# Performance work log

Hardware: AMD Instinct MI355X
Metric: run time of the kernel (lower is better)

The kernel has to match this reference:

```python
import jax, jax.numpy as jnp
import numpy as np


def setup_inputs() -> dict:
    key = jax.random.key(0)
    k1, k2 = jax.random.split(key)
    B, D, T = 32, 128, 1024   # batch, emb_dim, time (bdt layout)
    K = 4096                  # emb_size (codebook entries)
    x = jax.random.normal(k1, (B, D, T), dtype=jnp.float32)
    # nn.Embedding weight, init uniform(-1/K, 1/K) in the original; scale irrelevant for correctness
    W = jax.random.normal(k2, (K, D), dtype=jnp.float32) * (1.0 / K)
    return {"x": x, "W": W}


def reference(x, W):
    # Quantizer.forward with bdt_flag=True, eval mode (no EMA buffer update).
    # x: [B, D, T], W: [K, D] codebook
    xt = jnp.transpose(x, (0, 2, 1))            # [B, T, D]
    B, T, D = xt.shape
    flat = xt.reshape(-1, D)                    # [N, D]
    dist = (jnp.sum(W * W, axis=1)
            - 2.0 * flat @ W.T
            + jnp.sum(flat * flat, axis=1, keepdims=True))
    qidx = jnp.argmin(dist, axis=1).reshape(B, T)          # [B, T] int
    embed_idx = jnp.take(W, qidx, axis=0)                  # [B, T, D] == onehot @ W
    # straight-through estimator
    embed_idx_qx = xt + jax.lax.stop_gradient(embed_idx - xt)
    embed_idx_qx = jnp.transpose(embed_idx_qx, (0, 2, 1))  # back to [B, D, T]
    return embed_idx, embed_idx_qx, qidx
```

## Files before the change

kernel.cpp:

```cpp
#include <hip/hip_runtime.h>

typedef float    f4 __attribute__((ext_vector_type(4)));
typedef float    f2 __attribute__((ext_vector_type(2)));
typedef _Float16 h8 __attribute__((ext_vector_type(8)));

#define B_ 32
#define D_ 128
#define T_ 1024
#define K_ 4096
#define NROWS (B_ * T_)
#define LPX 132
#define INF_ 3.4e38f

#define SCHED_FENCE() __builtin_amdgcn_sched_barrier(0)
#define MFMA16 __builtin_amdgcn_mfma_f32_16x16x32_f16

__device__ __forceinline__ float opaquef(float x) { asm volatile("" : "+v"(x)); return x; }

__device__ float np_sumsq128(const float* a) {
  float r[8];
#pragma unroll
  for (int j = 0; j < 8; ++j) r[j] = opaquef(a[j] * a[j]);
#pragma unroll
  for (int i = 8; i < 128; i += 8) {
#pragma unroll
    for (int j = 0; j < 8; ++j) r[j] = r[j] + opaquef(a[i + j] * a[i + j]);
  }
  return ((r[0] + r[1]) + (r[2] + r[3])) + ((r[4] + r[5]) + (r[6] + r[7]));
}

__global__ void wsq_kernel(const float* __restrict__ W, float* __restrict__ wsq,
                           unsigned* __restrict__ maxwsq) {
  int k = blockIdx.x * blockDim.x + threadIdx.x;
  if (k < K_) {
    float s = np_sumsq128(W + (size_t)k * D_);
    wsq[k] = s;
    atomicMax(maxwsq, __float_as_uint(s));
  }
}

__global__ void wbf_prep_kernel(const float* __restrict__ W, _Float16* __restrict__ Wbf) {
  int e = blockIdx.x * 256 + threadIdx.x;
  int j = e & 7, lane = (e >> 3) & 63, kk = (e >> 9) & 3, ct = e >> 11;
  int code = (ct << 4) + (lane & 15);
  int k = (kk << 5) + (((lane >> 4) & 3) << 3) + j;
  Wbf[e] = (_Float16)(W[(size_t)code * D_ + k] * 4096.0f);
}

#define LDB(R0, R1, R2, R3, WQ)               \
  R0 = *(const h8*)(pwb);                     \
  R1 = *(const h8*)(pwb + 1024);              \
  R2 = *(const h8*)(pwb + 2048);              \
  R3 = *(const h8*)(pwb + 3072);              \
  WQ = *pwq;                                  \
  pwb += 4096; pwq += 16;

#define TOP3_UPD(T, J, U, KK)                                                  \
  do {                                                                         \
    bool c1 = (U) < m1[T][J], c2 = (U) < m2[T][J];                             \
    m3[T][J] = __builtin_amdgcn_fmed3f((U), m2[T][J], m3[T][J]);               \
    m2[T][J] = __builtin_amdgcn_fmed3f((U), m1[T][J], m2[T][J]);               \
    m1[T][J] = fminf((U), m1[T][J]);                                           \
    i2[T][J] = c1 ? i1[T][J] : (c2 ? (KK) : i2[T][J]);                         \
    i1[T][J] = c1 ? (KK) : i1[T][J];                                           \
  } while (0)

#define CONSUME_MIN(B0, B1, B2, B3, WQ, CT)                                    \
  do {                                                                         \
    f4 z = {0.f, 0.f, 0.f, 0.f};                                               \
    f4 A0 = MFMA16(afr0[0], B0, z, 0, 0, 0);                                   \
    A0 = MFMA16(afr0[1], B1, A0, 0, 0, 0);                                     \
    f4 A1 = MFMA16(afr0[2], B2, z, 0, 0, 0);                                   \
    A1 = MFMA16(afr0[3], B3, A1, 0, 0, 0);                                     \
    f4 C0 = MFMA16(afr1[0], B0, z, 0, 0, 0);                                   \
    C0 = MFMA16(afr1[1], B1, C0, 0, 0, 0);                                     \
    f4 C1 = MFMA16(afr1[2], B2, z, 0, 0, 0);                                   \
    C1 = MFMA16(afr1[3], B3, C1, 0, 0, 0);                                     \
    const int kk_ = ((CT) << 4) + cidx;                                        \
    _Pragma("unroll")                                                          \
    for (int j = 0; j < 4; ++j) {                                              \
      float u0 = __fmaf_rn(-4.8828125e-4f, A0[j] + A1[j], WQ);                 \
      TOP3_UPD(0, j, u0, kk_);                                                 \
      float u1 = __fmaf_rn(-4.8828125e-4f, C0[j] + C1[j], WQ);                 \
      TOP3_UPD(1, j, u1, kk_);                                                 \
    }                                                                          \
  } while (0)

__global__ __launch_bounds__(256) void filter_kernel(
    const float* __restrict__ x, const _Float16* __restrict__ Wbf,
    const float* __restrict__ wsq, const unsigned* __restrict__ maxwsq,
    float* __restrict__ xsq_g, int* __restrict__ cnt, int* __restrict__ cand,
    int* __restrict__ flags, int* __restrict__ nflag, int* __restrict__ flist) {
  __shared__ float xs[32][LPX];
  __shared__ float xsqs[32];
  __shared__ float umin_sh[32][4];
  const int tid = threadIdx.x;
  const int blkrow = blockIdx.x * 32;
  const int b = blockIdx.x >> 5, t0 = (blockIdx.x & 31) << 5;

  {
    int tt = tid & 31, d0 = (tid >> 5) * 16;
    for (int dd = 0; dd < 16; ++dd) {
      int d = d0 + dd;
      xs[tt][d] = x[((size_t)b * D_ + d) * T_ + t0 + tt];
    }
  }
  __syncthreads();
  if (tid < 32) {
    float s = np_sumsq128(&xs[tid][0]);
    xsqs[tid] = s;
    xsq_g[blkrow + tid] = s;
  }
  __syncthreads();

  const int w = tid >> 6, lane = tid & 63;
  const int cidx = lane & 15;
  const int q = lane >> 4;

  h8 afr0[4], afr1[4];
#pragma unroll
  for (int kk = 0; kk < 4; ++kk)
#pragma unroll
    for (int j = 0; j < 8; ++j) {
      int k = (kk << 5) + (q << 3) + j;
      afr0[kk][j] = (_Float16)xs[cidx][k];
      afr1[kk][j] = (_Float16)xs[16 + cidx][k];
    }

  const float mw = sqrtf(__uint_as_float(*maxwsq)) * 1.0001f;

  float m1[2][4], m2[2][4], m3[2][4];
  int   i1[2][4], i2[2][4];
#pragma unroll
  for (int t = 0; t < 2; ++t)
#pragma unroll
    for (int j = 0; j < 4; ++j) {
      m1[t][j] = INF_; m2[t][j] = INF_; m3[t][j] = INF_;
      i1[t][j] = 0x7fffffff; i2[t][j] = 0x7fffffff;
    }
  const int ct0 = w << 6;

  {
    const char*  pwb = (const char*)Wbf + (size_t)ct0 * 4096 + (size_t)lane * 16;
    const float* pwq = wsq + (ct0 << 4) + cidx;
    h8 p0, p1, p2, p3, n0, n1, n2, n3;
    float wqc, wqn;
    LDB(p0, p1, p2, p3, wqc)
    for (int s = 0; s < 32; ++s) {
      const int c = ct0 + s * 2;
      LDB(n0, n1, n2, n3, wqn)
      SCHED_FENCE();
      CONSUME_MIN(p0, p1, p2, p3, wqc, c);
      SCHED_FENCE();
      LDB(p0, p1, p2, p3, wqc)
      SCHED_FENCE();
      CONSUME_MIN(n0, n1, n2, n3, wqn, c + 1);
      SCHED_FENCE();
    }
  }

  float lim[2][4];
#pragma unroll
  for (int t = 0; t < 2; ++t)
#pragma unroll
    for (int j = 0; j < 4; ++j) {
      float m = m1[t][j];
#pragma unroll
      for (int mask = 1; mask < 16; mask <<= 1)
        m = fminf(m, __shfl_xor(m, mask));
      if (cidx == 0) umin_sh[t * 16 + (q << 2) + j][w] = m;
    }
  __syncthreads();
#pragma unroll
  for (int t = 0; t < 2; ++t)
#pragma unroll
    for (int j = 0; j < 4; ++j) {
      int rl = t * 16 + (q << 2) + j;
      float mg = fminf(fminf(umin_sh[rl][0], umin_sh[rl][1]),
                       fminf(umin_sh[rl][2], umin_sh[rl][3]));
      float xn = sqrtf(xsqs[rl]) * 1.0001f;
      lim[t][j] = mg + 2.2f * (0.002f * xn * mw) + 4e-5f;
    }

#pragma unroll
  for (int t = 0; t < 2; ++t)
#pragma unroll
    for (int j = 0; j < 4; ++j) {
      int row = blkrow + t * 16 + (q << 2) + j;
      bool ovf = false;
      if (m1[t][j] <= lim[t][j]) {
        int pos = atomicAdd(&cnt[row], 1);
        if (pos < 16) cand[(row << 4) + pos] = i1[t][j]; else ovf = true;
      }
      if (m2[t][j] <= lim[t][j]) {
        int pos = atomicAdd(&cnt[row], 1);
        if (pos < 16) cand[(row << 4) + pos] = i2[t][j]; else ovf = true;
      }
      if (ovf || m3[t][j] <= lim[t][j]) {
        int old = atomicOr(&flags[row], 1);
        if (old == 0) { int p = atomicAdd(nflag, 1); flist[p & (NROWS - 1)] = row; }
      }
    }
}

__global__ __launch_bounds__(256) void rescore_kernel(
    const float* __restrict__ x, const float* __restrict__ W,
    const float* __restrict__ wsq, const float* __restrict__ xsq,
    const int* __restrict__ cnt, const int* __restrict__ cand,
    const int* __restrict__ flags,
    int* __restrict__ qout, float* __restrict__ out2) {
  const int wid = threadIdx.x >> 6, lane = threadIdx.x & 63;
  const int r = blockIdx.x * 4 + wid;
  if (flags[r]) return;
  int c = cnt[r]; if (c > 16) c = 16;
  int best;
  if (c == 1) {
    best = cand[r << 4] & (K_ - 1);
  } else {
    const float* xr = x + ((size_t)(r >> 10) * D_) * T_ + (r & 1023);
    float v = INF_; int k = 0x7fffffff;
    if (lane < c) {
      k = cand[(r << 4) + lane] & (K_ - 1);
      const float* wr = W + (size_t)k * D_;
      float mm = 0.f;
#pragma unroll 16
      for (int d = 0; d < D_; ++d)
        mm = __fmaf_rn(xr[(size_t)d * T_], wr[d], mm);
      v = __fadd_rn(__fmaf_rn(-2.f, mm, wsq[k]), xsq[r]);
    }
#pragma unroll
    for (int mask = 1; mask < 16; mask <<= 1) {
      float vo = __shfl_xor(v, mask); int ko = __shfl_xor(k, mask);
      if (vo < v || (vo == v && ko < k)) { v = vo; k = ko; }
    }
    best = k & (K_ - 1);
  }
  if (lane == 0) { qout[r] = best; out2[r] = (float)best; }
}

__global__ __launch_bounds__(256) void exact_kernel(
    const float* __restrict__ x, const float* __restrict__ W,
    const float* __restrict__ wsq, const float* __restrict__ xsq,
    const int* __restrict__ nflag, const int* __restrict__ flist,
    unsigned long long* __restrict__ eslot) {
  __shared__ float xrow[128];
  __shared__ float wl[64][130];
  int n = *nflag; if (n > NROWS) n = NROWS;
  for (int item = blockIdx.x; item < n * 8; item += 256) {
    int r = flist[item >> 3] & (NROWS - 1);
    int chunk = item & 7;
    const float* xr = x + ((size_t)(r >> 10) * D_) * T_ + (r & 1023);
    __syncthreads();
    if (threadIdx.x < 128) xrow[threadIdx.x] = xr[(size_t)threadIdx.x * T_];
    float v = INF_; int kb = 0x7fffffff;
    for (int s = chunk * 8; s < chunk * 8 + 8; ++s) {
      __syncthreads();
      const f2* src = (const f2*)(W + (size_t)s * 64 * D_);
      for (int e = threadIdx.x; e < 4096; e += 256)
        *(f2*)&wl[e >> 6][(e & 63) * 2] = src[e];
      __syncthreads();
      if (threadIdx.x < 64) {
        int k = s * 64 + threadIdx.x;
        float mm = 0.f;
#pragma unroll 16
        for (int d = 0; d < D_; ++d)
          mm = __fmaf_rn(xrow[d], wl[threadIdx.x][d], mm);
        float vv = __fadd_rn(__fmaf_rn(-2.f, mm, wsq[k]), xsq[r]);
        if (vv < v) { v = vv; kb = k; }
      }
    }
    if (threadIdx.x < 64) {
#pragma unroll
      for (int mask = 1; mask < 64; mask <<= 1) {
        float vo = __shfl_xor(v, mask); int ko = __shfl_xor(kb, mask);
        if (vo < v || (vo == v && ko < kb)) { v = vo; kb = ko; }
      }
      if (threadIdx.x == 0) {
        unsigned long long pk =
            ((unsigned long long)__float_as_uint(v) << 32) | (unsigned)kb;
        atomicMin(&eslot[r], pk);
      }
    }
    __syncthreads();
  }
}

__global__ void finalize_kernel(const int* __restrict__ flags,
                                const unsigned long long* __restrict__ eslot,
                                int* __restrict__ qout, float* __restrict__ out2) {
  int r = blockIdx.x * 256 + threadIdx.x;
  if (flags[r]) {
    int best = (int)(unsigned)(eslot[r] & 0xFFFFFFFFull) & (K_ - 1);
    qout[r] = best; out2[r] = (float)best;
  }
}

__global__ void scatter0_kernel(const float* __restrict__ W,
                                const int* __restrict__ q,
                                float* __restrict__ out0) {
  int r = blockIdx.x * 2 + (threadIdx.x >> 7);
  int d = threadIdx.x & 127;
  int k = q[r] & (K_ - 1);
  out0[(size_t)r * D_ + d] = W[(size_t)k * D_ + d];
}

__global__ void scatter1_kernel(const float* __restrict__ W,
                                const int* __restrict__ q,
                                float* __restrict__ out1) {
  int b = blockIdx.x >> 7;
  int d = blockIdx.x & 127;
  for (int t = threadIdx.x; t < T_; t += 256) {
    int k = q[b * T_ + t] & (K_ - 1);
    out1[((size_t)b * D_ + d) * T_ + t] = W[(size_t)k * D_ + d];
  }
}

extern "C" void kernel_launch(void* const* d_in, const int* in_sizes, int n_in,
                              void* d_out, int out_size, void* d_ws, size_t ws_size,
                              hipStream_t stream) {
  const float* x = (const float*)d_in[0];
  const float* W = (const float*)d_in[1];
  float* out  = (float*)d_out;
  float* out0 = out;
  float* out1 = out + (size_t)NROWS * D_;
  float* out2 = out + 2 * (size_t)NROWS * D_;

  float*    wsq   = (float*)d_ws;
  float*    xsq   = (float*)((char*)d_ws + (16 << 10));
  int*      q     = (int*)((char*)d_ws + (144 << 10));
  int*      cnt   = (int*)((char*)d_ws + (272 << 10));
  unsigned* maxw  = (unsigned*)((char*)d_ws + (400 << 10));
  int*      flags = (int*)((char*)d_ws + (404 << 10));

  int*      cand  = (int*)out0;
  _Float16* Wbf   = (_Float16*)((char*)(void*)out0 + (2 << 20));
  int*      flist = (int*)((char*)(void*)out0 + (3 << 20));
  int*      nflag = (int*)((char*)(void*)out0 + (3 << 20) + (128 << 10));
  unsigned long long* eslot =
      (unsigned long long*)((char*)(void*)out0 + (3 << 20) + (256 << 10));

  hipMemsetAsync((char*)d_ws + (272 << 10), 0, (260 << 10) + 64, stream);
  hipMemsetAsync(nflag, 0, 64, stream);
  hipMemsetAsync(eslot, 0xFF, NROWS * sizeof(unsigned long long), stream);
  wsq_kernel<<<K_ / 256, 256, 0, stream>>>(W, wsq, maxw);
  wbf_prep_kernel<<<K_ * D_ / 256, 256, 0, stream>>>(W, Wbf);
  filter_kernel<<<NROWS / 32, 256, 0, stream>>>(x, Wbf, wsq, maxw, xsq,
                                                cnt, cand, flags, nflag, flist);
  rescore_kernel<<<NROWS / 4, 256, 0, stream>>>(x, W, wsq, xsq, cnt, cand, flags, q, out2);
  exact_kernel<<<256, 256, 0, stream>>>(x, W, wsq, xsq, nflag, flist, eslot);
  finalize_kernel<<<NROWS / 256, 256, 0, stream>>>(flags, eslot, q, out2);
  scatter0_kernel<<<NROWS / 2, 256, 0, stream>>>(W, q, out0);
  scatter1_kernel<<<B_ * D_, 256, 0, stream>>>(W, q, out1);
}
```

Measured before the change: 174.5 us.

## Software-pipeline MFMA chains against top-3 tracking and merge prep kernels

Restructures the filter kernel's main loop so the MFMA chain for one code tile is issued before the top-3 tracking of the previous tile. This overlaps matrix-unit latency with the VALU min-tracking work. The two independent partial accumulators are also merged into one serial chain per row group, which saves an add but lengthens the dependency chain. The wsq and fp16 codebook prep kernels are fused into one launch to save launch overhead, at the cost of more live accumulator registers.

```diff
diff --git a/kernel.cpp b/kernel.cpp
--- a/kernel.cpp
+++ b/kernel.cpp
@@ -29,22 +29,18 @@
   return ((r[0] + r[1]) + (r[2] + r[3])) + ((r[4] + r[5]) + (r[6] + r[7]));
 }
 
-__global__ void wsq_kernel(const float* __restrict__ W, float* __restrict__ wsq,
-                           unsigned* __restrict__ maxwsq) {
-  int k = blockIdx.x * blockDim.x + threadIdx.x;
-  if (k < K_) {
-    float s = np_sumsq128(W + (size_t)k * D_);
-    wsq[k] = s;
-    atomicMax(maxwsq, __float_as_uint(s));
-  }
-}
-
-__global__ void wbf_prep_kernel(const float* __restrict__ W, _Float16* __restrict__ Wbf) {
+__global__ void prep_kernel(const float* __restrict__ W, _Float16* __restrict__ Wbf,
+                            float* __restrict__ wsq, unsigned* __restrict__ maxwsq) {
   int e = blockIdx.x * 256 + threadIdx.x;
   int j = e & 7, lane = (e >> 3) & 63, kk = (e >> 9) & 3, ct = e >> 11;
   int code = (ct << 4) + (lane & 15);
   int k = (kk << 5) + (((lane >> 4) & 3) << 3) + j;
   Wbf[e] = (_Float16)(W[(size_t)code * D_ + k] * 4096.0f);
+  if (e < K_) {
+    float s = np_sumsq128(W + (size_t)e * D_);
+    wsq[e] = s;
+    atomicMax(maxwsq, __float_as_uint(s));
+  }
 }
 
 #define LDB(R0, R1, R2, R3, WQ)               \
@@ -65,23 +61,27 @@
     i1[T][J] = c1 ? (KK) : i1[T][J];                                           \
   } while (0)
 
-#define CONSUME_MIN(B0, B1, B2, B3, WQ, CT)                                    \
+#define MFMACHAIN(ACC0, ACC1, B0, B1, B2, B3)        \
+  do {                                               \
+    f4 z = {0.f, 0.f, 0.f, 0.f};                     \
+    ACC0 = MFMA16(afr0[0], B0, z, 0, 0, 0);          \
+    ACC0 = MFMA16(afr0[1], B1, ACC0, 0, 0, 0);       \
+    ACC0 = MFMA16(afr0[2], B2, ACC0, 0, 0, 0);       \
+    ACC0 = MFMA16(afr0[3], B3, ACC0, 0, 0, 0);       \
+    ACC1 = MFMA16(afr1[0], B0, z, 0, 0, 0);          \
+    ACC1 = MFMA16(afr1[1], B1, ACC1, 0, 0, 0);       \
+    ACC1 = MFMA16(afr1[2], B2, ACC1, 0, 0, 0);       \
+    ACC1 = MFMA16(afr1[3], B3, ACC1, 0, 0, 0);       \
+  } while (0)
+
+#define TRACK(ACC0, ACC1, WQ, CT)                                              \
   do {                                                                         \
-    f4 z = {0.f, 0.f, 0.f, 0.f};                                               \
-    f4 A0 = MFMA16(afr0[0], B0, z, 0, 0, 0);                                   \
-    A0 = MFMA16(afr0[1], B1, A0, 0, 0, 0);                                     \
-    f4 A1 = MFMA16(afr0[2], B2, z, 0, 0, 0);                                   \
-    A1 = MFMA16(afr0[3], B3, A1, 0, 0, 0);                                     \
-    f4 C0 = MFMA16(afr1[0], B0, z, 0, 0, 0);                                   \
-    C0 = MFMA16(afr1[1], B1, C0, 0, 0, 0);                                     \
-    f4 C1 = MFMA16(afr1[2], B2, z, 0, 0, 0);                                   \
-    C1 = MFMA16(afr1[3], B3, C1, 0, 0, 0);                                     \
     const int kk_ = ((CT) << 4) + cidx;                                        \
     _Pragma("unroll")                                                          \
     for (int j = 0; j < 4; ++j) {                                              \
-      float u0 = __fmaf_rn(-4.8828125e-4f, A0[j] + A1[j], WQ);                 \
+      float u0 = __fmaf_rn(-4.8828125e-4f, ACC0[j], WQ);                       \
       TOP3_UPD(0, j, u0, kk_);                                                 \
-      float u1 = __fmaf_rn(-4.8828125e-4f, C0[j] + C1[j], WQ);                 \
+      float u1 = __fmaf_rn(-4.8828125e-4f, ACC1[j], WQ);                       \
       TOP3_UPD(1, j, u1, kk_);                                                 \
     }                                                                          \
   } while (0)
@@ -143,20 +143,35 @@
   {
     const char*  pwb = (const char*)Wbf + (size_t)ct0 * 4096 + (size_t)lane * 16;
     const float* pwq = wsq + (ct0 << 4) + cidx;
-    h8 p0, p1, p2, p3, n0, n1, n2, n3;
-    float wqc, wqn;
-    LDB(p0, p1, p2, p3, wqc)
-    for (int s = 0; s < 32; ++s) {
+    h8 bA0, bA1, bA2, bA3, bB0, bB1, bB2, bB3;
+    float wqA, wqB;
+    f4 aA0, aA1, aB0, aB1;
+    LDB(bA0, bA1, bA2, bA3, wqA)
+    SCHED_FENCE();
+    MFMACHAIN(aA0, aA1, bA0, bA1, bA2, bA3);
+    SCHED_FENCE();
+    for (int s = 0; s < 31; ++s) {
       const int c = ct0 + s * 2;
-      LDB(n0, n1, n2, n3, wqn)
-      SCHED_FENCE();
-      CONSUME_MIN(p0, p1, p2, p3, wqc, c);
-      SCHED_FENCE();
-      LDB(p0, p1, p2, p3, wqc)
-      SCHED_FENCE();
-      CONSUME_MIN(n0, n1, n2, n3, wqn, c + 1);
-      SCHED_FENCE();
-    }
+      LDB(bB0, bB1, bB2, bB3, wqB)
+      SCHED_FENCE();
+      MFMACHAIN(aB0, aB1, bB0, bB1, bB2, bB3);
+      SCHED_FENCE();
+      TRACK(aA0, aA1, wqA, c);
+      SCHED_FENCE();
+      LDB(bA0, bA1, bA2, bA3, wqA)
+      SCHED_FENCE();
+      MFMACHAIN(aA0, aA1, bA0, bA1, bA2, bA3);
+      SCHED_FENCE();
+      TRACK(aB0, aB1, wqB, c + 1);
+      SCHED_FENCE();
+    }
+    LDB(bB0, bB1, bB2, bB3, wqB)
+    SCHED_FENCE();
+    MFMACHAIN(aB0, aB1, bB0, bB1, bB2, bB3);
+    SCHED_FENCE();
+    TRACK(aA0, aA1, wqA, ct0 + 62);
+    SCHED_FENCE();
+    TRACK(aB0, aB1, wqB, ct0 + 63);
   }
 
   float lim[2][4];
@@ -342,8 +357,7 @@
   hipMemsetAsync((char*)d_ws + (272 << 10), 0, (260 << 10) + 64, stream);
   hipMemsetAsync(nflag, 0, 64, stream);
   hipMemsetAsync(eslot, 0xFF, NROWS * sizeof(unsigned long long), stream);
-  wsq_kernel<<<K_ / 256, 256, 0, stream>>>(W, wsq, maxw);
-  wbf_prep_kernel<<<K_ * D_ / 256, 256, 0, stream>>>(W, Wbf);
+  prep_kernel<<<K_ * D_ / 256, 256, 0, stream>>>(W, Wbf, wsq, maxw);
   filter_kernel<<<NROWS / 32, 256, 0, stream>>>(x, Wbf, wsq, maxw, xsq,
                                                 cnt, cand, flags, nflag, flist);
   rescore_kernel<<<NROWS / 4, 256, 0, stream>>>(x, W, wsq, xsq, cnt, cand, flags, q, out2);
```

Measured after the change: 191.5 us. 1.1x slower.
